# Kernel tuning notes

Hardware: AMD Instinct MI355X
Metric: run time of the kernel (lower is better)

The kernel has to match this reference:

```python
import jax, jax.numpy as jnp
import numpy as np

TAU = 2.0
V_TH = 0.5
BN_EPS = 1e-5
SG_ALPHA = 4.0  # spikingjelly sigmoid surrogate default

@jax.custom_vjp
def heaviside(x):
    return (x >= 0.0).astype(x.dtype)

def _hv_fwd(x):
    return heaviside(x), x

def _hv_bwd(x, g):
    s = jax.nn.sigmoid(SG_ALPHA * x)
    return (g * SG_ALPHA * s * (1.0 - s),)

heaviside.defvjp(_hv_fwd, _hv_bwd)

def lif(x):
    """Multi-step LIF (decay_input=True, v_reset=0, hard reset, detach_reset).
    x: [T, ...] -> spikes [T, ...]"""
    def step(v, xt):
        v = v + (xt - v) / TAU          # charge
        s = heaviside(v - V_TH)          # fire
        v = v * (1.0 - jax.lax.stop_gradient(s))  # hard reset (detached)
        return v, s
    _, spikes = jax.lax.scan(step, jnp.zeros_like(x[0]), x)
    return spikes

def conv1x1(x, w):
    # x: [T,B,C,H,W], w: [Cout,Cin]
    return jnp.einsum('oc,tbchw->tbohw', w, x)

def bn(x, g, b, m, v):
    inv = g / jnp.sqrt(v + BN_EPS)
    return (x - m[None, None, :, None, None]) * inv[None, None, :, None, None] + b[None, None, :, None, None]

def setup_inputs() -> dict:
    key = jax.random.key(0)
    ks = jax.random.split(key, 16)
    T, B, C, H, W = 4, 32, 384, 16, 16
    heads = 8
    sc = 1.0 / np.sqrt(C)
    d = {}
    d['x'] = jax.random.normal(ks[0], (T, B, C, H, W), jnp.float32)
    d['q_w'] = jax.random.normal(ks[1], (C, C), jnp.float32) * sc
    d['k_w'] = jax.random.normal(ks[2], (C, C), jnp.float32) * sc
    d['v_w'] = jax.random.normal(ks[3], (C, C), jnp.float32) * sc
    for i, p in enumerate(['q', 'k', 'v', 'p']):
        kk = jax.random.split(ks[4 + i], 4)
        d[p + '_g'] = 1.0 + 0.1 * jax.random.normal(kk[0], (C,), jnp.float32)
        d[p + '_b'] = 0.1 * jax.random.normal(kk[1], (C,), jnp.float32)
        d[p + '_m'] = 0.1 * jax.random.normal(kk[2], (C,), jnp.float32)
        d[p + '_v'] = jax.random.uniform(kk[3], (C,), jnp.float32, 0.5, 1.5)
    d['th_w'] = jax.random.normal(ks[8], (heads, heads), jnp.float32) / np.sqrt(heads)
    d['proj_w'] = jax.random.normal(ks[9], (C, C), jnp.float32) * sc
    d['proj_bias'] = 0.1 * jax.random.normal(ks[10], (C,), jnp.float32)
    return d

NUM_HEADS = 8

def reference(x, q_w, k_w, v_w,
              q_g, q_b, q_m, q_v,
              k_g, k_b, k_m, k_v,
              v_g, v_b, v_m, v_v,
              p_g, p_b, p_m, p_v,
              th_w, proj_w, proj_bias):
    T, B, C, H, W = x.shape
    N = H * W
    hd = C // NUM_HEADS
    identity = x
    xs = lif(x)  # shortcut_lif

    def branch(w, g, b, m, vv):
        return lif(bn(conv1x1(xs, w), g, b, m, vv))  # [T,B,C,H,W] spikes

    def to_heads(t):
        # [T,B,C,H,W] -> [T,B,heads,N,hd]  (flatten(3).transpose(-1,-2).reshape.permute)
        return t.reshape(T, B, C, N).transpose(0, 1, 3, 2).reshape(T, B, N, NUM_HEADS, hd).transpose(0, 1, 3, 2, 4)

    q = to_heads(branch(q_w, q_g, q_b, q_m, q_v))
    k = to_heads(branch(k_w, k_g, k_b, k_m, k_v))
    v = to_heads(branch(v_w, v_g, v_b, v_m, v_v))

    kv = (k * v).sum(axis=3)                      # [T,B,heads,hd]
    kv = jnp.einsum('oh,tbhd->tbod', th_w, kv)    # talking heads (Conv1d k=1, no bias)
    kv = lif(kv)[:, :, :, None, :]                # [T,B,heads,1,hd]

    x_att = q * kv                                # [T,B,heads,N,hd]
    # transpose(3,4).reshape(T,B,C,H,W): [T,B,heads,hd,N] -> channels = heads*hd
    x_att = x_att.transpose(0, 1, 2, 4, 3).reshape(T, B, C, H, W)

    x_out = conv1x1(x_att, proj_w) + proj_bias[None, None, :, None, None]
    x_out = bn(x_out, p_g, p_b, p_m, p_v)
    x_out = x_out + identity
    return (x_out, v)
```

## Files before the change

### kernel.cpp

```cpp
#include <hip/hip_runtime.h>
#include <math.h>

typedef int i32x4 __attribute__((ext_vector_type(4)));
typedef unsigned long long u64;

constexpr int TT = 4;
constexpr int BB = 32;
constexpr int CC = 384;
constexpr int NN = 256;
constexpr int HEADS = 8;
constexpr int HD = 48;
constexpr int BCN = BB * CC * NN;
constexpr int TBCN = TT * BCN;
constexpr int CCC = CC * CC;
constexpr float MARGIN = 1e-4f;
constexpr unsigned FCAP = 262144;

struct __align__(16) LdsB {
    unsigned char W[2][3][64][64];
    unsigned char S[2][4][32][64];
    unsigned char R[4][32][64];
};
struct __align__(16) LdsP {
    unsigned char W[2][3][64][64];
    unsigned char S[2][4][32][64];
};

__global__ __launch_bounds__(256) void k_wsplit(
    const float* __restrict__ qw, const float* __restrict__ kw,
    const float* __restrict__ vw, const float* __restrict__ pw,
    signed char* __restrict__ wq, unsigned* __restrict__ cnt) {
    if (blockIdx.x == 0 && threadIdx.x == 0) *cnt = 0u;
    int idx = blockIdx.x * 256 + threadIdx.x;
    int mat = idx / CCC, r = idx % CCC;
    const float* src = (mat == 0) ? qw : (mat == 1) ? kw : (mat == 2) ? vw : pw;
    double w = (double)src[r];
    long long W = llround(w * 8388608.0);
    signed char d0 = (signed char)(W & 0xff); W = (W - d0) >> 8;
    signed char d1 = (signed char)(W & 0xff); W = (W - d1) >> 8;
    signed char d2 = (signed char)W;
    size_t base = (size_t)mat * 3 * CCC;
    wq[base + 0 * CCC + r] = d0;
    wq[base + 1 * CCC + r] = d1;
    wq[base + 2 * CCC + r] = d2;
}

__global__ __launch_bounds__(256) void k_lif_x(const float* __restrict__ x,
                                               unsigned char* __restrict__ xs) {
    __shared__ unsigned char sL[4][64][64];
    const int b_ = blockIdx.x, c0 = blockIdx.y * 64, n0 = blockIdx.z * 64;
    const int tid = threadIdx.x;

    float vm[4][4];
#pragma unroll
    for (int a = 0; a < 4; ++a)
#pragma unroll
        for (int j = 0; j < 4; ++j) vm[a][j] = 0.f;

#pragma unroll
    for (int t = 0; t < TT; ++t) {
#pragma unroll
        for (int a = 0; a < 4; ++a) {
            int idx = tid + 256 * a;
            int ci = idx >> 4, nj4 = idx & 15;
            float4 xv = *(const float4*)&x[((size_t)((t * BB + b_) * CC) + c0 + ci) * NN + n0 + nj4 * 4];
            float xa[4] = {xv.x, xv.y, xv.z, xv.w};
#pragma unroll
            for (int j = 0; j < 4; ++j) {
                vm[a][j] = __fadd_rn(vm[a][j], __fmul_rn(__fsub_rn(xa[j], vm[a][j]), 0.5f));
                int s = (vm[a][j] >= 0.5f);
                sL[t][nj4 * 4 + j][ci] = (unsigned char)s;
                if (s) vm[a][j] = 0.f;
            }
        }
    }
    __syncthreads();
#pragma unroll
    for (int i = 0; i < 16; ++i) {
        int s = tid + 256 * i;
        int c4 = s & 15, n = (s >> 4) & 63, t = s >> 10;
        *(uchar4*)&xs[((size_t)((t * BB + b_) * NN) + n0 + n) * CC + c0 + c4 * 4] =
            *(const uchar4*)&sL[t][n][c4 * 4];
    }
}

__global__ __launch_bounds__(256, 2) void k_branch_i8(
    const unsigned char* __restrict__ xs, const signed char* __restrict__ wq0,
    const float* __restrict__ qg, const float* __restrict__ qb,
    const float* __restrict__ qm, const float* __restrict__ qv,
    const float* __restrict__ kg_, const float* __restrict__ kb_,
    const float* __restrict__ km_, const float* __restrict__ kv_,
    const float* __restrict__ vg, const float* __restrict__ vb,
    const float* __restrict__ vm_, const float* __restrict__ vv_,
    unsigned char* __restrict__ qs, unsigned char* __restrict__ ks,
    unsigned char* __restrict__ vs,
    unsigned* __restrict__ cnt, unsigned* __restrict__ list) {
    __shared__ LdsB L;
    const int b_ = blockIdx.x;
    const int mat = blockIdx.y / 6, ob = (blockIdx.y % 6) * 64, nb = blockIdx.z * 32;
    const int tid = threadIdx.x, lane = tid & 63, w = tid >> 6;
    const int lo16 = lane & 15, hi4 = lane >> 4;

    const signed char* wq = wq0 + (size_t)mat * 3 * CCC;
    const float* gg  = (mat == 0) ? qg : (mat == 1) ? kg_ : vg;
    const float* bbp = (mat == 0) ? qb : (mat == 1) ? kb_ : vb;
    const float* mmp = (mat == 0) ? qm : (mat == 1) ? km_ : vm_;
    const float* vvp = (mat == 0) ? qv : (mat == 1) ? kv_ : vv_;
    unsigned char* spk = (mat == 0) ? qs : (mat == 1) ? ks : vs;

    const int wo = tid >> 2, wc16 = tid & 3;
    const size_t wroff = (size_t)(ob + wo) * CC + wc16 * 16;
    const int e0 = tid, e1 = tid + 256;
    const int t0 = e0 >> 7, n0_ = (e0 >> 2) & 31, c0_ = e0 & 3;
    const int t1 = e1 >> 7, n1_ = (e1 >> 2) & 31, c1_ = e1 & 3;
    const size_t sr0 = ((size_t)((t0 * BB + b_) * NN) + nb + n0_) * CC + c0_ * 16;
    const size_t sr1 = ((size_t)((t1 * BB + b_) * NN) + nb + n1_) * CC + c1_ * 16;

    i32x4 acc[3][4][2];
#pragma unroll
    for (int p = 0; p < 3; ++p)
#pragma unroll
        for (int t = 0; t < 4; ++t)
#pragma unroll
            for (int nf = 0; nf < 2; ++nf) acc[p][t][nf] = (i32x4){0, 0, 0, 0};

    i32x4 rw0, rw1, rw2, rs0, rs1;
    auto LOAD = [&](int k0) {
        rw0 = *(const i32x4*)&wq[0 * CCC + wroff + k0];
        rw1 = *(const i32x4*)&wq[1 * CCC + wroff + k0];
        rw2 = *(const i32x4*)&wq[2 * CCC + wroff + k0];
        rs0 = *(const i32x4*)&xs[sr0 + k0];
        rs1 = *(const i32x4*)&xs[sr1 + k0];
    };
    auto STORE = [&](int buf) {
        *(i32x4*)&L.W[buf][0][wo][wc16 * 16] = rw0;
        *(i32x4*)&L.W[buf][1][wo][wc16 * 16] = rw1;
        *(i32x4*)&L.W[buf][2][wo][wc16 * 16] = rw2;
        *(i32x4*)&L.S[buf][t0][n0_][c0_ * 16] = rs0;
        *(i32x4*)&L.S[buf][t1][n1_][c1_ * 16] = rs1;
    };

    LOAD(0);
    STORE(0);
    int cur = 0;
    for (int s = 0; s < 6; ++s) {
        __syncthreads();
        if (s < 5) LOAD((s + 1) * 64);
        i32x4 af0 = *(const i32x4*)&L.W[cur][0][w * 16 + lo16][hi4 * 16];
        i32x4 af1 = *(const i32x4*)&L.W[cur][1][w * 16 + lo16][hi4 * 16];
        i32x4 af2 = *(const i32x4*)&L.W[cur][2][w * 16 + lo16][hi4 * 16];
#pragma unroll
        for (int t = 0; t < 4; ++t)
#pragma unroll
            for (int nf = 0; nf < 2; ++nf) {
                i32x4 bfr = *(const i32x4*)&L.S[cur][t][nf * 16 + lo16][hi4 * 16];
                acc[0][t][nf] = __builtin_amdgcn_mfma_i32_16x16x64_i8(af0, bfr, acc[0][t][nf], 0, 0, 0);
                acc[1][t][nf] = __builtin_amdgcn_mfma_i32_16x16x64_i8(af1, bfr, acc[1][t][nf], 0, 0, 0);
                acc[2][t][nf] = __builtin_amdgcn_mfma_i32_16x16x64_i8(af2, bfr, acc[2][t][nf], 0, 0, 0);
            }
        if (s < 5) STORE(cur ^ 1);
        cur ^= 1;
    }

#pragma unroll
    for (int r = 0; r < 4; ++r) {
        const int o = ob + w * 16 + hi4 * 4 + r;
        const float inv = __fdiv_rn(gg[o], __fsqrt_rn(__fadd_rn(vvp[o], 1e-5f)));
        const float mu = mmp[o], be = bbp[o];
#pragma unroll
        for (int nf = 0; nf < 2; ++nf) {
            float vmem = 0.f, mg = 1e9f;
#pragma unroll
            for (int t = 0; t < 4; ++t) {
                long long N = (long long)acc[0][t][nf][r] + 256LL * acc[1][t][nf][r]
                            + 65536LL * acc[2][t][nf][r];
                float dotf = (float)((double)N * 0x1p-23);
                float y = __fadd_rn(__fmul_rn(__fsub_rn(dotf, mu), inv), be);
                vmem = __fadd_rn(vmem, __fmul_rn(__fsub_rn(y, vmem), 0.5f));
                mg = fminf(mg, fabsf(__fsub_rn(vmem, 0.5f)));
                int s = (vmem >= 0.5f);
                L.R[t][nf * 16 + lo16][w * 16 + hi4 * 4 + r] = (unsigned char)s;
                if (s) vmem = 0.f;
            }
            if (mg < MARGIN) {
                unsigned idx = atomicAdd(cnt, 1u);
                int n = nb + nf * 16 + lo16;
                if (idx < FCAP) list[idx] = ((unsigned)mat << 22) | ((unsigned)b_ << 17) |
                                            ((unsigned)o << 8) | (unsigned)n;
            }
        }
    }
    __syncthreads();
#pragma unroll
    for (int i = 0; i < 8; ++i) {
        int e = tid + 256 * i;
        int c4 = e & 15, n = (e >> 4) & 31, t = e >> 9;
        *(uchar4*)&spk[((size_t)((t * BB + b_) * NN) + nb + n) * CC + ob + c4 * 4] =
            *(const uchar4*)&L.R[t][n][c4 * 4];
    }
}

__global__ __launch_bounds__(256) void k_fixup(
    const unsigned char* __restrict__ xs,
    const float* __restrict__ qw, const float* __restrict__ kw, const float* __restrict__ vw,
    const float* __restrict__ qg, const float* __restrict__ qb,
    const float* __restrict__ qm, const float* __restrict__ qv,
    const float* __restrict__ kg_, const float* __restrict__ kb_,
    const float* __restrict__ km_, const float* __restrict__ kv_,
    const float* __restrict__ vg, const float* __restrict__ vb,
    const float* __restrict__ vm_, const float* __restrict__ vv_,
    unsigned char* __restrict__ qs, unsigned char* __restrict__ ks,
    unsigned char* __restrict__ vs,
    const unsigned* __restrict__ cnt, const unsigned* __restrict__ list) {
    __shared__ __align__(16) float sw[CC];
    __shared__ __align__(16) unsigned char sx[TT][CC];
    __shared__ float dots[TT];
    unsigned nfl = *cnt;
    if (nfl > FCAP) nfl = FCAP;
    for (unsigned i = blockIdx.x; i < nfl; i += gridDim.x) {
        unsigned e = list[i];
        int mat = e >> 22, b_ = (e >> 17) & 31, o = (e >> 8) & 511, n = e & 255;
        const float* wbase = (mat == 0) ? qw : (mat == 1) ? kw : vw;
        const float* wrow = wbase + (size_t)o * CC;
        for (int c = threadIdx.x; c < CC; c += 256) sw[c] = wrow[c];
        if (threadIdx.x < TT * (CC / 8)) {
            int t = threadIdx.x / (CC / 8), q = threadIdx.x % (CC / 8);
            *(u64*)&sx[t][q * 8] =
                *(const u64*)&xs[((size_t)((t * BB + b_) * NN) + n) * CC + q * 8];
        }
        __syncthreads();
        if (threadIdx.x < TT) {
            int t = threadIdx.x;
            float acc = 0.f;
            for (int c = 0; c < CC; ++c)
                acc = __fmaf_rn((float)sx[t][c], sw[c], acc);
            dots[t] = acc;
        }
        __syncthreads();
        if (threadIdx.x == 0) {
            const float* G = (mat == 0) ? qg : (mat == 1) ? kg_ : vg;
            const float* Bb = (mat == 0) ? qb : (mat == 1) ? kb_ : vb;
            const float* M = (mat == 0) ? qm : (mat == 1) ? km_ : vm_;
            const float* V = (mat == 0) ? qv : (mat == 1) ? kv_ : vv_;
            unsigned char* S = (mat == 0) ? qs : (mat == 1) ? ks : vs;
            const float inv = __fdiv_rn(G[o], __fsqrt_rn(__fadd_rn(V[o], 1e-5f)));
            const float mu = M[o], be = Bb[o];
            float vmem = 0.f;
            for (int t = 0; t < TT; ++t) {
                float y = __fadd_rn(__fmul_rn(__fsub_rn(dots[t], mu), inv), be);
                vmem = __fadd_rn(vmem, __fmul_rn(__fsub_rn(y, vmem), 0.5f));
                int s = (vmem >= 0.5f);
                S[((size_t)((t * BB + b_) * NN) + n) * CC + o] = (unsigned char)s;
                if (s) vmem = 0.f;
            }
        }
        __syncthreads();
    }
}

__global__ __launch_bounds__(256) void k_vout(const unsigned char* __restrict__ vs,
                                              float* __restrict__ vout) {
    int e = blockIdx.x * 256 + threadIdx.x;
    int d4 = e % 12;
    int r = e / 12;
    int n = r & 255;
    r >>= 8;
    int h = r & 7;
    int tb = r >> 3;
    uchar4 u = *(const uchar4*)&vs[((size_t)tb * NN + n) * CC + h * HD + d4 * 4];
    float4 o = {(float)u.x, (float)u.y, (float)u.z, (float)u.w};
    *(float4*)&vout[(((size_t)tb * HEADS + h) * NN + n) * HD + d4 * 4] = o;
}

__global__ __launch_bounds__(256) void k_kvsum(const unsigned char* __restrict__ ks,
                                               const unsigned char* __restrict__ vs,
                                               int* __restrict__ kvsum) {
    __shared__ int P[5][CC];
    const int tb = blockIdx.x, tid = threadIdx.x;
    if (tid < 240) {
        int c8 = tid % 48, sl = tid / 48;
        int a[8] = {0, 0, 0, 0, 0, 0, 0, 0};
        for (int n = sl; n < NN; n += 5) {
            u64 kk = *(const u64*)&ks[((size_t)tb * NN + n) * CC + c8 * 8];
            u64 vvv = *(const u64*)&vs[((size_t)tb * NN + n) * CC + c8 * 8];
            u64 u = kk & vvv;
#pragma unroll
            for (int j = 0; j < 8; ++j) a[j] += (int)((u >> (8 * j)) & 1);
        }
#pragma unroll
        for (int j = 0; j < 8; ++j) P[sl][c8 * 8 + j] = a[j];
    }
    __syncthreads();
    for (int c = tid; c < CC; c += 256) {
        kvsum[(size_t)tb * CC + c] = P[0][c] + P[1][c] + P[2][c] + P[3][c] + P[4][c];
    }
}

__global__ __launch_bounds__(384) void k_thlif(const int* __restrict__ kvsum,
                                               const float* __restrict__ th,
                                               unsigned char* __restrict__ kvm) {
    __shared__ int kv0[TT][CC];
    const int b_ = blockIdx.x, c = threadIdx.x;
#pragma unroll
    for (int t = 0; t < TT; ++t) kv0[t][c] = kvsum[(size_t)(t * BB + b_) * CC + c];
    __syncthreads();
    const int ho = c / HD, d = c % HD;
    float vmem = 0.f;
#pragma unroll
    for (int t = 0; t < TT; ++t) {
        float s = 0.f;
#pragma unroll
        for (int h = 0; h < HEADS; ++h)
            s = __fadd_rn(s, __fmul_rn(th[ho * HEADS + h], (float)kv0[t][h * HD + d]));
        vmem = __fadd_rn(vmem, __fmul_rn(__fsub_rn(s, vmem), 0.5f));
        int sp = (vmem >= 0.5f);
        kvm[(size_t)(t * BB + b_) * CC + c] = (unsigned char)sp;
        if (sp) vmem = 0.f;
    }
}

__global__ __launch_bounds__(256, 2) void k_proj_i8(
    const unsigned char* __restrict__ qs, const unsigned char* __restrict__ kvm,
    const signed char* __restrict__ wq, const float* __restrict__ pbias,
    const float* __restrict__ gg, const float* __restrict__ bbp,
    const float* __restrict__ mmp, const float* __restrict__ vvp,
    const float* __restrict__ xin, float* __restrict__ out) {
    __shared__ LdsP L;
    const int b_ = blockIdx.x, ob = blockIdx.y * 64, nb = blockIdx.z * 32;
    const int tid = threadIdx.x, lane = tid & 63, w = tid >> 6;
    const int lo16 = lane & 15, hi4 = lane >> 4;

    const int wo = tid >> 2, wc16 = tid & 3;
    const size_t wroff = (size_t)(ob + wo) * CC + wc16 * 16;
    const int e0 = tid, e1 = tid + 256;
    const int t0 = e0 >> 7, n0_ = (e0 >> 2) & 31, c0_ = e0 & 3;
    const int t1 = e1 >> 7, n1_ = (e1 >> 2) & 31, c1_ = e1 & 3;
    const size_t sr0 = ((size_t)((t0 * BB + b_) * NN) + nb + n0_) * CC + c0_ * 16;
    const size_t sr1 = ((size_t)((t1 * BB + b_) * NN) + nb + n1_) * CC + c1_ * 16;
    const size_t mr0 = (size_t)((t0 * BB + b_) * CC) + c0_ * 16;
    const size_t mr1 = (size_t)((t1 * BB + b_) * CC) + c1_ * 16;

    i32x4 acc[3][4][2];
#pragma unroll
    for (int p = 0; p < 3; ++p)
#pragma unroll
        for (int t = 0; t < 4; ++t)
#pragma unroll
            for (int nf = 0; nf < 2; ++nf) acc[p][t][nf] = (i32x4){0, 0, 0, 0};

    i32x4 rw0, rw1, rw2, rs0, rs1;
    auto LOAD = [&](int k0) {
        rw0 = *(const i32x4*)&wq[0 * CCC + wroff + k0];
        rw1 = *(const i32x4*)&wq[1 * CCC + wroff + k0];
        rw2 = *(const i32x4*)&wq[2 * CCC + wroff + k0];
        i32x4 q0 = *(const i32x4*)&qs[sr0 + k0];
        i32x4 m0 = *(const i32x4*)&kvm[mr0 + k0];
        i32x4 q1 = *(const i32x4*)&qs[sr1 + k0];
        i32x4 m1 = *(const i32x4*)&kvm[mr1 + k0];
        rs0 = q0 & m0;
        rs1 = q1 & m1;
    };
    auto STORE = [&](int buf) {
        *(i32x4*)&L.W[buf][0][wo][wc16 * 16] = rw0;
        *(i32x4*)&L.W[buf][1][wo][wc16 * 16] = rw1;
        *(i32x4*)&L.W[buf][2][wo][wc16 * 16] = rw2;
        *(i32x4*)&L.S[buf][t0][n0_][c0_ * 16] = rs0;
        *(i32x4*)&L.S[buf][t1][n1_][c1_ * 16] = rs1;
    };

    LOAD(0);
    STORE(0);
    int cur = 0;
    for (int s = 0; s < 6; ++s) {
        __syncthreads();
        if (s < 5) LOAD((s + 1) * 64);
        i32x4 af0 = *(const i32x4*)&L.W[cur][0][w * 16 + lo16][hi4 * 16];
        i32x4 af1 = *(const i32x4*)&L.W[cur][1][w * 16 + lo16][hi4 * 16];
        i32x4 af2 = *(const i32x4*)&L.W[cur][2][w * 16 + lo16][hi4 * 16];
#pragma unroll
        for (int t = 0; t < 4; ++t)
#pragma unroll
            for (int nf = 0; nf < 2; ++nf) {
                i32x4 bfr = *(const i32x4*)&L.S[cur][t][nf * 16 + lo16][hi4 * 16];
                acc[0][t][nf] = __builtin_amdgcn_mfma_i32_16x16x64_i8(af0, bfr, acc[0][t][nf], 0, 0, 0);
                acc[1][t][nf] = __builtin_amdgcn_mfma_i32_16x16x64_i8(af1, bfr, acc[1][t][nf], 0, 0, 0);
                acc[2][t][nf] = __builtin_amdgcn_mfma_i32_16x16x64_i8(af2, bfr, acc[2][t][nf], 0, 0, 0);
            }
        if (s < 5) STORE(cur ^ 1);
        cur ^= 1;
    }

#pragma unroll
    for (int r = 0; r < 4; ++r) {
        const int o = ob + w * 16 + hi4 * 4 + r;
        const double inv = (double)gg[o] / sqrt((double)vvp[o] + 1e-5);
        const double mu = (double)mmp[o], be = (double)bbp[o], pb = (double)pbias[o];
#pragma unroll
        for (int nf = 0; nf < 2; ++nf) {
#pragma unroll
            for (int t = 0; t < 4; ++t) {
                long long N = (long long)acc[0][t][nf][r] + 256LL * acc[1][t][nf][r]
                            + 65536LL * acc[2][t][nf][r];
                double tot = (double)N * 0x1p-23;
                size_t idx = ((size_t)((t * BB + b_) * CC) + o) * NN + nb + nf * 16 + lo16;
                double y = (tot + pb - mu) * inv + be;
                out[idx] = (float)(y + (double)xin[idx]);
            }
        }
    }
}

extern "C" void kernel_launch(void* const* d_in, const int* in_sizes, int n_in,
                              void* d_out, int out_size, void* d_ws, size_t ws_size,
                              hipStream_t stream) {
    const float* x    = (const float*)d_in[0];
    const float* q_w  = (const float*)d_in[1];
    const float* k_w  = (const float*)d_in[2];
    const float* v_w  = (const float*)d_in[3];
    const float* q_g  = (const float*)d_in[4];
    const float* q_b  = (const float*)d_in[5];
    const float* q_m  = (const float*)d_in[6];
    const float* q_v  = (const float*)d_in[7];
    const float* k_g  = (const float*)d_in[8];
    const float* k_b  = (const float*)d_in[9];
    const float* k_m  = (const float*)d_in[10];
    const float* k_v  = (const float*)d_in[11];
    const float* v_g  = (const float*)d_in[12];
    const float* v_b  = (const float*)d_in[13];
    const float* v_m  = (const float*)d_in[14];
    const float* v_v  = (const float*)d_in[15];
    const float* p_g  = (const float*)d_in[16];
    const float* p_b  = (const float*)d_in[17];
    const float* p_m  = (const float*)d_in[18];
    const float* p_v  = (const float*)d_in[19];
    const float* th_w = (const float*)d_in[20];
    const float* pr_w = (const float*)d_in[21];
    const float* pr_b = (const float*)d_in[22];

    float* out  = (float*)d_out;
    float* vout = out + (size_t)TBCN;

    unsigned char* ws  = (unsigned char*)d_ws;
    unsigned char* xs  = ws;
    unsigned char* qs  = ws + (size_t)TBCN;
    unsigned char* ks2 = ws + (size_t)2 * TBCN;
    unsigned char* vs2 = ws + (size_t)3 * TBCN;
    signed char* wq    = (signed char*)(ws + (size_t)4 * TBCN);
    int* kvsum         = (int*)(ws + (size_t)4 * TBCN + 12ull * CCC);
    unsigned char* kvm = (unsigned char*)(kvsum + TT * BB * CC);
    unsigned* fcnt     = (unsigned*)(kvm + (size_t)TT * BB * CC + 64);
    unsigned* flist    = fcnt + 16;

    k_wsplit<<<(4 * CCC) / 256, 256, 0, stream>>>(q_w, k_w, v_w, pr_w, wq, fcnt);
    k_lif_x<<<dim3(BB, CC / 64, NN / 64), 256, 0, stream>>>(x, xs);

    k_branch_i8<<<dim3(BB, 18, NN / 32), 256, 0, stream>>>(
        xs, wq,
        q_g, q_b, q_m, q_v,
        k_g, k_b, k_m, k_v,
        v_g, v_b, v_m, v_v,
        qs, ks2, vs2, fcnt, flist);

    k_fixup<<<2048, 256, 0, stream>>>(xs, q_w, k_w, v_w,
                                      q_g, q_b, q_m, q_v,
                                      k_g, k_b, k_m, k_v,
                                      v_g, v_b, v_m, v_v,
                                      qs, ks2, vs2, fcnt, flist);

    k_vout<<<(TBCN / 4) / 256, 256, 0, stream>>>(vs2, vout);
    k_kvsum<<<TT * BB, 256, 0, stream>>>(ks2, vs2, kvsum);
    k_thlif<<<BB, CC, 0, stream>>>(kvsum, th_w, kvm);

    k_proj_i8<<<dim3(BB, CC / 64, NN / 32), 256, 0, stream>>>(
        qs, kvm, wq + 3ull * 3 * CCC, pr_b,
        p_g, p_b, p_m, p_v, x, out);
}
```

Measured before the change: 167.3 us.

## XOR-swizzle LDS tiles in int8 GEMMs and fuse v float output into branch kernel

Applies an XOR swizzle to the 16-byte column slots of the weight and spike LDS tiles in both int8 MFMA kernels, so that row-strided fragment reads no longer hit the same LDS banks. The float v output is now written directly from the branch kernel's epilogue, and from the fixup kernel for corrected entries. This removes the separate k_vout pass that re-read the v spikes. The fused writes are scalar and only partly coalesced, which may cost some store efficiency.

```diff
diff --git a/kernel.cpp b/kernel.cpp
--- a/kernel.cpp
+++ b/kernel.cpp
@@ -93,13 +93,14 @@
     const float* __restrict__ vg, const float* __restrict__ vb,
     const float* __restrict__ vm_, const float* __restrict__ vv_,
     unsigned char* __restrict__ qs, unsigned char* __restrict__ ks,
-    unsigned char* __restrict__ vs,
+    unsigned char* __restrict__ vs, float* __restrict__ vout,
     unsigned* __restrict__ cnt, unsigned* __restrict__ list) {
     __shared__ LdsB L;
     const int b_ = blockIdx.x;
     const int mat = blockIdx.y / 6, ob = (blockIdx.y % 6) * 64, nb = blockIdx.z * 32;
     const int tid = threadIdx.x, lane = tid & 63, w = tid >> 6;
     const int lo16 = lane & 15, hi4 = lane >> 4;
+    const int xsw = (lo16 >> 1) & 3;
 
     const signed char* wq = wq0 + (size_t)mat * 3 * CCC;
     const float* gg  = (mat == 0) ? qg : (mat == 1) ? kg_ : vg;
@@ -109,10 +110,13 @@
     unsigned char* spk = (mat == 0) ? qs : (mat == 1) ? ks : vs;
 
     const int wo = tid >> 2, wc16 = tid & 3;
+    const int wsl = (wc16 ^ ((wo >> 1) & 3)) * 16;
     const size_t wroff = (size_t)(ob + wo) * CC + wc16 * 16;
     const int e0 = tid, e1 = tid + 256;
     const int t0 = e0 >> 7, n0_ = (e0 >> 2) & 31, c0_ = e0 & 3;
     const int t1 = e1 >> 7, n1_ = (e1 >> 2) & 31, c1_ = e1 & 3;
+    const int sl0 = (c0_ ^ ((n0_ >> 1) & 3)) * 16;
+    const int sl1 = (c1_ ^ ((n1_ >> 1) & 3)) * 16;
     const size_t sr0 = ((size_t)((t0 * BB + b_) * NN) + nb + n0_) * CC + c0_ * 16;
     const size_t sr1 = ((size_t)((t1 * BB + b_) * NN) + nb + n1_) * CC + c1_ * 16;
 
@@ -133,11 +137,11 @@
         rs1 = *(const i32x4*)&xs[sr1 + k0];
     };
     auto STORE = [&](int buf) {
-        *(i32x4*)&L.W[buf][0][wo][wc16 * 16] = rw0;
-        *(i32x4*)&L.W[buf][1][wo][wc16 * 16] = rw1;
-        *(i32x4*)&L.W[buf][2][wo][wc16 * 16] = rw2;
-        *(i32x4*)&L.S[buf][t0][n0_][c0_ * 16] = rs0;
-        *(i32x4*)&L.S[buf][t1][n1_][c1_ * 16] = rs1;
+        *(i32x4*)&L.W[buf][0][wo][wsl] = rw0;
+        *(i32x4*)&L.W[buf][1][wo][wsl] = rw1;
+        *(i32x4*)&L.W[buf][2][wo][wsl] = rw2;
+        *(i32x4*)&L.S[buf][t0][n0_][sl0] = rs0;
+        *(i32x4*)&L.S[buf][t1][n1_][sl1] = rs1;
     };
 
     LOAD(0);
@@ -146,14 +150,14 @@
     for (int s = 0; s < 6; ++s) {
         __syncthreads();
         if (s < 5) LOAD((s + 1) * 64);
-        i32x4 af0 = *(const i32x4*)&L.W[cur][0][w * 16 + lo16][hi4 * 16];
-        i32x4 af1 = *(const i32x4*)&L.W[cur][1][w * 16 + lo16][hi4 * 16];
-        i32x4 af2 = *(const i32x4*)&L.W[cur][2][w * 16 + lo16][hi4 * 16];
+        i32x4 af0 = *(const i32x4*)&L.W[cur][0][w * 16 + lo16][(hi4 ^ xsw) * 16];
+        i32x4 af1 = *(const i32x4*)&L.W[cur][1][w * 16 + lo16][(hi4 ^ xsw) * 16];
+        i32x4 af2 = *(const i32x4*)&L.W[cur][2][w * 16 + lo16][(hi4 ^ xsw) * 16];
 #pragma unroll
         for (int t = 0; t < 4; ++t)
 #pragma unroll
             for (int nf = 0; nf < 2; ++nf) {
-                i32x4 bfr = *(const i32x4*)&L.S[cur][t][nf * 16 + lo16][hi4 * 16];
+                i32x4 bfr = *(const i32x4*)&L.S[cur][t][nf * 16 + lo16][(hi4 ^ xsw) * 16];
                 acc[0][t][nf] = __builtin_amdgcn_mfma_i32_16x16x64_i8(af0, bfr, acc[0][t][nf], 0, 0, 0);
                 acc[1][t][nf] = __builtin_amdgcn_mfma_i32_16x16x64_i8(af1, bfr, acc[1][t][nf], 0, 0, 0);
                 acc[2][t][nf] = __builtin_amdgcn_mfma_i32_16x16x64_i8(af2, bfr, acc[2][t][nf], 0, 0, 0);
@@ -195,8 +199,17 @@
     for (int i = 0; i < 8; ++i) {
         int e = tid + 256 * i;
         int c4 = e & 15, n = (e >> 4) & 31, t = e >> 9;
-        *(uchar4*)&spk[((size_t)((t * BB + b_) * NN) + nb + n) * CC + ob + c4 * 4] =
-            *(const uchar4*)&L.R[t][n][c4 * 4];
+        uchar4 s4 = *(const uchar4*)&L.R[t][n][c4 * 4];
+        *(uchar4*)&spk[((size_t)((t * BB + b_) * NN) + nb + n) * CC + ob + c4 * 4] = s4;
+        if (mat == 2) {
+            const unsigned char* sp = (const unsigned char*)&s4;
+#pragma unroll
+            for (int j = 0; j < 4; ++j) {
+                int c = ob + c4 * 4 + j;
+                int h = c / HD, d = c % HD;
+                vout[(((size_t)(t * BB + b_) * HEADS + h) * NN + nb + n) * HD + d] = (float)sp[j];
+            }
+        }
     }
 }
 
@@ -210,7 +223,7 @@
     const float* __restrict__ vg, const float* __restrict__ vb,
     const float* __restrict__ vm_, const float* __restrict__ vv_,
     unsigned char* __restrict__ qs, unsigned char* __restrict__ ks,
-    unsigned char* __restrict__ vs,
+    unsigned char* __restrict__ vs, float* __restrict__ vout,
     const unsigned* __restrict__ cnt, const unsigned* __restrict__ list) {
     __shared__ __align__(16) float sw[CC];
     __shared__ __align__(16) unsigned char sx[TT][CC];
@@ -251,25 +264,15 @@
                 vmem = __fadd_rn(vmem, __fmul_rn(__fsub_rn(y, vmem), 0.5f));
                 int s = (vmem >= 0.5f);
                 S[((size_t)((t * BB + b_) * NN) + n) * CC + o] = (unsigned char)s;
+                if (mat == 2) {
+                    int h = o / HD, d = o % HD;
+                    vout[(((size_t)(t * BB + b_) * HEADS + h) * NN + n) * HD + d] = (float)s;
+                }
                 if (s) vmem = 0.f;
             }
         }
         __syncthreads();
     }
-}
-
-__global__ __launch_bounds__(256) void k_vout(const unsigned char* __restrict__ vs,
-                                              float* __restrict__ vout) {
-    int e = blockIdx.x * 256 + threadIdx.x;
-    int d4 = e % 12;
-    int r = e / 12;
-    int n = r & 255;
-    r >>= 8;
-    int h = r & 7;
-    int tb = r >> 3;
-    uchar4 u = *(const uchar4*)&vs[((size_t)tb * NN + n) * CC + h * HD + d4 * 4];
-    float4 o = {(float)u.x, (float)u.y, (float)u.z, (float)u.w};
-    *(float4*)&vout[(((size_t)tb * HEADS + h) * NN + n) * HD + d4 * 4] = o;
 }
 
 __global__ __launch_bounds__(256) void k_kvsum(const unsigned char* __restrict__ ks,
@@ -329,12 +332,16 @@
     const int b_ = blockIdx.x, ob = blockIdx.y * 64, nb = blockIdx.z * 32;
     const int tid = threadIdx.x, lane = tid & 63, w = tid >> 6;
     const int lo16 = lane & 15, hi4 = lane >> 4;
+    const int xsw = (lo16 >> 1) & 3;
 
     const int wo = tid >> 2, wc16 = tid & 3;
+    const int wsl = (wc16 ^ ((wo >> 1) & 3)) * 16;
     const size_t wroff = (size_t)(ob + wo) * CC + wc16 * 16;
     const int e0 = tid, e1 = tid + 256;
     const int t0 = e0 >> 7, n0_ = (e0 >> 2) & 31, c0_ = e0 & 3;
     const int t1 = e1 >> 7, n1_ = (e1 >> 2) & 31, c1_ = e1 & 3;
+    const int sl0 = (c0_ ^ ((n0_ >> 1) & 3)) * 16;
+    const int sl1 = (c1_ ^ ((n1_ >> 1) & 3)) * 16;
     const size_t sr0 = ((size_t)((t0 * BB + b_) * NN) + nb + n0_) * CC + c0_ * 16;
     const size_t sr1 = ((size_t)((t1 * BB + b_) * NN) + nb + n1_) * CC + c1_ * 16;
     const size_t mr0 = (size_t)((t0 * BB + b_) * CC) + c0_ * 16;
@@ -361,11 +368,11 @@
         rs1 = q1 & m1;
     };
     auto STORE = [&](int buf) {
-        *(i32x4*)&L.W[buf][0][wo][wc16 * 16] = rw0;
-        *(i32x4*)&L.W[buf][1][wo][wc16 * 16] = rw1;
-        *(i32x4*)&L.W[buf][2][wo][wc16 * 16] = rw2;
-        *(i32x4*)&L.S[buf][t0][n0_][c0_ * 16] = rs0;
-        *(i32x4*)&L.S[buf][t1][n1_][c1_ * 16] = rs1;
+        *(i32x4*)&L.W[buf][0][wo][wsl] = rw0;
+        *(i32x4*)&L.W[buf][1][wo][wsl] = rw1;
+        *(i32x4*)&L.W[buf][2][wo][wsl] = rw2;
+        *(i32x4*)&L.S[buf][t0][n0_][sl0] = rs0;
+        *(i32x4*)&L.S[buf][t1][n1_][sl1] = rs1;
     };
 
     LOAD(0);
@@ -374,14 +381,14 @@
     for (int s = 0; s < 6; ++s) {
         __syncthreads();
         if (s < 5) LOAD((s + 1) * 64);
-        i32x4 af0 = *(const i32x4*)&L.W[cur][0][w * 16 + lo16][hi4 * 16];
-        i32x4 af1 = *(const i32x4*)&L.W[cur][1][w * 16 + lo16][hi4 * 16];
-        i32x4 af2 = *(const i32x4*)&L.W[cur][2][w * 16 + lo16][hi4 * 16];
+        i32x4 af0 = *(const i32x4*)&L.W[cur][0][w * 16 + lo16][(hi4 ^ xsw) * 16];
+        i32x4 af1 = *(const i32x4*)&L.W[cur][1][w * 16 + lo16][(hi4 ^ xsw) * 16];
+        i32x4 af2 = *(const i32x4*)&L.W[cur][2][w * 16 + lo16][(hi4 ^ xsw) * 16];
 #pragma unroll
         for (int t = 0; t < 4; ++t)
 #pragma unroll
             for (int nf = 0; nf < 2; ++nf) {
-                i32x4 bfr = *(const i32x4*)&L.S[cur][t][nf * 16 + lo16][hi4 * 16];
+                i32x4 bfr = *(const i32x4*)&L.S[cur][t][nf * 16 + lo16][(hi4 ^ xsw) * 16];
                 acc[0][t][nf] = __builtin_amdgcn_mfma_i32_16x16x64_i8(af0, bfr, acc[0][t][nf], 0, 0, 0);
                 acc[1][t][nf] = __builtin_amdgcn_mfma_i32_16x16x64_i8(af1, bfr, acc[1][t][nf], 0, 0, 0);
                 acc[2][t][nf] = __builtin_amdgcn_mfma_i32_16x16x64_i8(af2, bfr, acc[2][t][nf], 0, 0, 0);
@@ -459,15 +466,14 @@
         q_g, q_b, q_m, q_v,
         k_g, k_b, k_m, k_v,
         v_g, v_b, v_m, v_v,
-        qs, ks2, vs2, fcnt, flist);
+        qs, ks2, vs2, vout, fcnt, flist);
 
     k_fixup<<<2048, 256, 0, stream>>>(xs, q_w, k_w, v_w,
                                       q_g, q_b, q_m, q_v,
                                       k_g, k_b, k_m, k_v,
                                       v_g, v_b, v_m, v_v,
-                                      qs, ks2, vs2, fcnt, flist);
-
-    k_vout<<<(TBCN / 4) / 256, 256, 0, stream>>>(vs2, vout);
+                                      qs, ks2, vs2, vout, fcnt, flist);
+
     k_kvsum<<<TT * BB, 256, 0, stream>>>(ks2, vs2, kvsum);
     k_thlif<<<BB, CC, 0, stream>>>(kvsum, th_w, kvm);
 
```

Measured after the change: 171.5 us. 2.5% more time.
